# Optimization experiments

Measured on AMD Instinct MI355X. Metric: run time of the kernel, lower is better.

## Reference

```python
import jax, jax.numpy as jnp
import numpy as np
import math

B, S, D = 4, 1024, 1024
H, DK, DV = 16, 64, 64
MAX_REL = 32  # use_neg_dist=True -> vocab = 2*MAX_REL+1


def setup_inputs() -> dict:
    key = jax.random.key(0)
    ks = jax.random.split(key, 13)
    sc = 0.02
    return {
        "key": jax.random.normal(ks[0], (B, S, D), jnp.float32),
        "value": jax.random.normal(ks[1], (B, S, D), jnp.float32),
        "query": jax.random.normal(ks[2], (B, S, D), jnp.float32),
        "Wk": jax.random.normal(ks[3], (D, H * DK), jnp.float32) * sc,
        "bk": jnp.zeros((H * DK,), jnp.float32),
        "Wq": jax.random.normal(ks[4], (D, H * DK), jnp.float32) * sc,
        "bq": jnp.zeros((H * DK,), jnp.float32),
        "Wv": jax.random.normal(ks[5], (D, H * DV), jnp.float32) * sc,
        "bv": jnp.zeros((H * DV,), jnp.float32),
        "Wo": jax.random.normal(ks[6], (H * DV, D), jnp.float32) * sc,
        "bo": jnp.zeros((D,), jnp.float32),
        "emb_k": jax.random.normal(ks[7], (2 * MAX_REL + 1, DK), jnp.float32) * sc,
        "emb_v": jax.random.normal(ks[8], (2 * MAX_REL + 1, DV), jnp.float32) * sc,
    }


def reference(key, value, query, Wk, bk, Wq, bq, Wv, bv, Wo, bo, emb_k, emb_v):
    # project and split heads -> [B, H, S, d]
    def shape(x, d):
        return x.reshape(B, S, H, d).transpose(0, 2, 1, 3)

    k = shape(key @ Wk + bk, DK)
    v = shape(value @ Wv + bv, DV)
    q = shape(query @ Wq + bq, DK)

    # relative position ids: [S, S] in [0, 2*MAX_REL]
    r = jnp.arange(S)
    rel_idx = jnp.clip(r[None, :] - r[:, None], -MAX_REL, MAX_REL) + MAX_REL
    rel_k = emb_k[rel_idx]  # [S, S, DK]
    rel_v = emb_v[rel_idx]  # [S, S, DV]

    q = q / math.sqrt(DK)
    # content scores + relative-key scores (relative_matmul with transpose=True)
    scores = jnp.einsum("bhqd,bhkd->bhqk", q, k) + jnp.einsum("bhqd,qkd->bhqk", q, rel_k)
    attn = jax.nn.softmax(scores.astype(jnp.float32), axis=-1).astype(q.dtype)

    # context + relative-value contribution (relative_matmul with transpose=False)
    ctx = jnp.einsum("bhqk,bhkd->bhqd", attn, v) + jnp.einsum("bhqk,qkd->bhqd", attn, rel_v)
    ctx = ctx.transpose(0, 2, 1, 3).reshape(B, S, H * DV)
    final_output = ctx @ Wo + bo
    return final_output, attn
```

## Files before the change

kernel.cpp:

```cpp
#include <hip/hip_runtime.h>
#include <hip/hip_bf16.h>

#define B_ 4
#define S_ 1024
#define D_ 1024
#define H_ 16

typedef unsigned short u16;
typedef __bf16 bf16x8 __attribute__((ext_vector_type(8)));
typedef float f32x4 __attribute__((ext_vector_type(4)));

__device__ inline u16 f2bf(float f) {
    __bf16 h = (__bf16)f;
    return __builtin_bit_cast(u16, h);
}
__device__ inline float bf2f(u16 u) {
    unsigned int x = ((unsigned int)u) << 16;
    return __builtin_bit_cast(float, x);
}
__device__ inline void gl_lds16(const u16* g, u16* lbase) {
    __builtin_amdgcn_global_load_lds(
        (const __attribute__((address_space(1))) unsigned int*)g,
        (__attribute__((address_space(3))) unsigned int*)lbase, 16, 0, 0);
}
__device__ inline bf16x8 frag_swz(const u16* lds, int row, int chunk) {
    int off = (row << 6) + ((chunk ^ (row & 7)) << 3);
    return *(const bf16x8*)(lds + off);
}
__device__ inline bf16x8 frag_p(const u16* lds, int row, int chunk) {
    int off = row * 72 + (chunk << 3);
    return *(const bf16x8*)(lds + off);
}
__device__ inline f32x4 mfma16(bf16x8 a, bf16x8 b, f32x4 c) {
    return __builtin_amdgcn_mfma_f32_16x16x32_bf16(a, b, c, 0, 0, 0);
}
__device__ inline void bar() {
    asm volatile("s_waitcnt lgkmcnt(0)\n\ts_barrier" ::: "memory");
}
__device__ inline void wait_vm0() {
    asm volatile("s_waitcnt vmcnt(0)" ::: "memory");
    __builtin_amdgcn_sched_barrier(0);
}
__device__ inline void wait_vm4() {
    asm volatile("s_waitcnt vmcnt(4)" ::: "memory");
    __builtin_amdgcn_sched_barrier(0);
}
__device__ inline void wait_vm8() {
    asm volatile("s_waitcnt vmcnt(8)" ::: "memory");
    __builtin_amdgcn_sched_barrier(0);
}
__device__ inline void wait_vm16() {
    asm volatile("s_waitcnt vmcnt(16)" ::: "memory");
    __builtin_amdgcn_sched_barrier(0);
}
__device__ inline void wait_vm20() {
    asm volatile("s_waitcnt vmcnt(20)" ::: "memory");
    __builtin_amdgcn_sched_barrier(0);
}
__device__ inline void wait_lgkm0() {
    asm volatile("s_waitcnt lgkmcnt(0)" ::: "memory");
    __builtin_amdgcn_sched_barrier(0);
}

__global__ __launch_bounds__(256) void cast_bf16_kernel(const float* __restrict__ src,
                                                        u16* __restrict__ dst, int n) {
    int i = (blockIdx.x * 256 + threadIdx.x) * 4;
    if (i >= n) return;
    float4 v = *(const float4*)(src + i);
    ushort4 o;
    o.x = f2bf(v.x); o.y = f2bf(v.y); o.z = f2bf(v.z); o.w = f2bf(v.w);
    *(ushort4*)(dst + i) = o;
}

__global__ __launch_bounds__(256) void tcast_kernel(const float* __restrict__ src,
                                                    u16* __restrict__ dst) {
    __shared__ float tile[32][33];
    int bx = blockIdx.x, by = blockIdx.y;
    int tx = threadIdx.x, ty = threadIdx.y;
    int x = bx * 32 + tx;
    for (int i = ty; i < 32; i += 8)
        tile[i][tx] = src[(size_t)(by * 32 + i) * 1024 + x];
    __syncthreads();
    int col = by * 32 + tx;
    for (int i = ty; i < 32; i += 8)
        dst[(size_t)(bx * 32 + i) * 1024 + col] = f2bf(tile[tx][i]);
}

__device__ inline void gemm_core(const u16* __restrict__ A, const u16* __restrict__ Bt,
                                 int m0, int n0, u16* lsA, u16* lsB, f32x4 acc[4][4]) {
    int tid = threadIdx.x, lane = tid & 63, wave = tid >> 6;
    int quad = lane >> 4, l16 = lane & 15;
    int wm = wave >> 1, wn = wave & 1;
    f32x4 z = {0.0f, 0.0f, 0.0f, 0.0f};
    for (int mi = 0; mi < 4; mi++)
        for (int ni = 0; ni < 4; ni++) acc[mi][ni] = z;
    auto stg = [&](int k0, int b) {
        const u16* abase = A + (size_t)m0 * 1024 + k0;
        const u16* bbase = Bt + (size_t)n0 * 1024 + k0;
#pragma unroll
        for (int j = 0; j < 4; j++) {
            int C = (wave * 4 + j) * 64 + lane;
            int row = C >> 3, c = C & 7;
            int sw = (c ^ (row & 7)) << 3;
            gl_lds16(abase + (size_t)row * 1024 + sw, lsA + b * 8192 + (wave * 4 + j) * 512);
            gl_lds16(bbase + (size_t)row * 1024 + sw, lsB + b * 8192 + (wave * 4 + j) * 512);
        }
    };
    stg(0, 0);
#pragma unroll 1
    for (int it = 0; it < 16; it++) {
        if (it < 15) {
            stg((it + 1) * 64, (it + 1) & 1);
            wait_vm8();
        } else {
            wait_vm0();
        }
        bar();
        const u16* cA = lsA + (it & 1) * 8192;
        const u16* cB = lsB + (it & 1) * 8192;
        for (int s = 0; s < 2; s++) {
            bf16x8 af[4], bfv[4];
            for (int mi = 0; mi < 4; mi++) af[mi] = frag_swz(cA, wm * 64 + mi * 16 + l16, s * 4 + quad);
            for (int ni = 0; ni < 4; ni++) bfv[ni] = frag_swz(cB, wn * 64 + ni * 16 + l16, s * 4 + quad);
            for (int mi = 0; mi < 4; mi++)
                for (int ni = 0; ni < 4; ni++)
                    acc[mi][ni] = mfma16(af[mi], bfv[ni], acc[mi][ni]);
        }
        bar();
    }
}

__global__ __launch_bounds__(256) void gemm_proj_kernel(
    const u16* __restrict__ xq, const u16* __restrict__ xk, const u16* __restrict__ xv,
    const u16* __restrict__ wt,
    const float* __restrict__ bq, const float* __restrict__ bk, const float* __restrict__ bv,
    u16* __restrict__ qb, u16* __restrict__ kb, u16* __restrict__ vtb) {
    __shared__ __align__(16) u16 lsA[2 * 128 * 64];
    __shared__ __align__(16) u16 lsB[2 * 128 * 64];
    int bid = blockIdx.x;
    int which = bid >> 8;
    int t = bid & 255;
    int m0 = (t >> 3) * 128, n0 = (t & 7) * 128;
    const u16* A = which == 0 ? xq : (which == 1 ? xk : xv);
    const u16* Bt = wt + (size_t)which * 1024 * 1024;
    const float* bias = which == 0 ? bq : (which == 1 ? bk : bv);
    f32x4 acc[4][4];
    gemm_core(A, Bt, m0, n0, lsA, lsB, acc);
    int tid = threadIdx.x, lane = tid & 63, wave = tid >> 6;
    int quad = lane >> 4, l16 = lane & 15;
    int wm = wave >> 1, wn = wave & 1;
    for (int mi = 0; mi < 4; mi++) {
        int rbase = m0 + wm * 64 + mi * 16 + quad * 4;
        int b = rbase >> 10, s0 = rbase & 1023;
        for (int ni = 0; ni < 4; ni++) {
            int n = n0 + wn * 64 + ni * 16 + l16;
            int h = n >> 6, d = n & 63;
            float bsv = bias[n];
            if (which == 2) {
                ushort4 pk;
                pk.x = f2bf(acc[mi][ni][0] + bsv);
                pk.y = f2bf(acc[mi][ni][1] + bsv);
                pk.z = f2bf(acc[mi][ni][2] + bsv);
                pk.w = f2bf(acc[mi][ni][3] + bsv);
                *(ushort4*)(vtb + ((size_t)(b * H_ + h) * 64 + d) * 1024 + s0) = pk;
            } else {
                u16* outp = (which == 0) ? qb : kb;
                float scl = (which == 0) ? 0.125f : 1.0f;
                for (int r = 0; r < 4; r++) {
                    int s = s0 + r;
                    outp[((size_t)(b * H_ + h) * 1024 + s) * 64 + d] = f2bf((acc[mi][ni][r] + bsv) * scl);
                }
            }
        }
    }
}

__global__ __launch_bounds__(256) void gemm_final_kernel(const u16* __restrict__ ctxb,
                                                         const u16* __restrict__ wot,
                                                         const float* __restrict__ bo,
                                                         float* __restrict__ out) {
    __shared__ __align__(16) u16 lsA[2 * 128 * 64];
    __shared__ __align__(16) u16 lsB[2 * 128 * 64];
    int bid = blockIdx.x;
    int m0 = (bid >> 3) * 128, n0 = (bid & 7) * 128;
    f32x4 acc[4][4];
    gemm_core(ctxb, wot, m0, n0, lsA, lsB, acc);
    int tid = threadIdx.x, lane = tid & 63, wave = tid >> 6;
    int quad = lane >> 4, l16 = lane & 15;
    int wm = wave >> 1, wn = wave & 1;
    for (int mi = 0; mi < 4; mi++)
        for (int ni = 0; ni < 4; ni++) {
            int n = n0 + wn * 64 + ni * 16 + l16;
            float bsv = bo[n];
            for (int r = 0; r < 4; r++) {
                int row = m0 + wm * 64 + mi * 16 + quad * 4 + r;
                out[(size_t)row * 1024 + n] = acc[mi][ni][r] + bsv;
            }
        }
}

__global__ __launch_bounds__(256, 2) void attn_kernel(
    const u16* __restrict__ qb, const u16* __restrict__ kb, const u16* __restrict__ vtb,
    const float* __restrict__ emb_k, const float* __restrict__ emb_v,
    float* __restrict__ attn_out, u16* __restrict__ ctxb) {
    __shared__ __align__(16) u16 kvbuf[4][64 * 64];
    __shared__ __align__(16) u16 pbuf[64 * 72];
    __shared__ __align__(16) u16 wqbuf[64 * 72];
    __shared__ __align__(16) u16 qrel[64 * 68];

    int bid = blockIdx.x;
    int qt = bid & 15, bh = bid >> 4;
    int tid = threadIdx.x, lane = tid & 63, wave = tid >> 6;
    int quad = lane >> 4, l16 = lane & 15;
    int mrow = wave * 16;

    const u16* qbase = qb + ((size_t)bh * 1024 + qt * 64) * 64;
    const u16* kbh = kb + (size_t)bh * 1024 * 64;
    const u16* vbh = vtb + (size_t)bh * 64 * 1024;

    auto stage = [&](const u16* src, int srcStride, u16* dst) {
#pragma unroll
        for (int j = 0; j < 2; j++) {
            int C = (wave * 2 + j) * 64 + lane;
            int row = C >> 3, c = C & 7;
            gl_lds16(src + (size_t)row * srcStride + ((c ^ (row & 7)) << 3),
                     dst + (wave * 2 + j) * 512);
        }
    };
    auto stage128 = [&](const u16* src, u16* dst) {
#pragma unroll
        for (int j = 0; j < 4; j++) {
            int C = (wave * 4 + j) * 64 + lane;
            int row = C >> 3, c = C & 7;
            gl_lds16(src + (size_t)row * 64 + ((c ^ (row & 7)) << 3),
                     dst + (wave * 4 + j) * 512);
        }
    };

    stage(qbase, 64, wqbuf);
    for (int i = tid; i < 65 * 64; i += 256) {
        int j = i >> 6, d = i & 63;
        pbuf[(j << 6) + ((((d >> 3) ^ (j & 7)) << 3) | (d & 7))] = f2bf(emb_k[i]);
    }
    wait_vm0();
    bar();

    {
        bf16x8 a0 = frag_swz(wqbuf, mrow + l16, quad);
        bf16x8 a1 = frag_swz(wqbuf, mrow + l16, 4 + quad);
#pragma unroll
        for (int ni = 0; ni < 5; ni++) {
            int rr = ni * 16 + l16;
            rr = rr > 64 ? 64 : rr;
            f32x4 a = {0.0f, 0.0f, 0.0f, 0.0f};
            a = mfma16(a0, frag_swz(pbuf, rr, quad), a);
            a = mfma16(a1, frag_swz(pbuf, rr, 4 + quad), a);
            int j = ni * 16 + l16;
            if (j < 65) {
#pragma unroll
                for (int r = 0; r < 4; r++)
                    qrel[(mrow + quad * 4 + r) * 68 + j] = f2bf(a[r]);
            }
        }
    }
    bf16x8 aq0 = frag_swz(wqbuf, mrow + l16, quad);
    bf16x8 aq1 = frag_swz(wqbuf, mrow + l16, 4 + quad);
    bar();

    float rel_l[4], rel_r[4];
#pragma unroll
    for (int r = 0; r < 4; r++) {
        int ql = mrow + quad * 4 + r;
        rel_l[r] = bf2f(qrel[ql * 68 + 0]);
        rel_r[r] = bf2f(qrel[ql * 68 + 64]);
    }
    stage128(kbh, kvbuf[0]);
    {
        unsigned int* wz = (unsigned int*)wqbuf;
        for (int i = lane; i < 16 * 36; i += 64) wz[mrow * 36 + i] = 0u;
    }

    float l_acc[4] = {0.0f, 0.0f, 0.0f, 0.0f};

#pragma unroll 1
    for (int it = 0; it < 8; it++) {
        if (it < 7) {
            stage128(kbh + (size_t)(it + 1) * 8192, (it & 1) ? kvbuf[0] : kvbuf[2]);
            wait_vm4();
        } else {
            wait_vm0();
        }
        bar();
        const u16* kl = (it & 1) ? kvbuf[2] : kvbuf[0];
        int cls = (it * 128 + 127 <= qt * 64 - 32) ? 0 : ((it * 128 >= qt * 64 + 95) ? 2 : 1);
        if (cls == 0) {
#pragma unroll
            for (int ni = 0; ni < 8; ni++) {
                f32x4 a = {0.0f, 0.0f, 0.0f, 0.0f};
                a = mfma16(aq0, frag_swz(kl, ni * 16 + l16, quad), a);
                a = mfma16(aq1, frag_swz(kl, ni * 16 + l16, 4 + quad), a);
#pragma unroll
                for (int r = 0; r < 4; r++) l_acc[r] += __expf(a[r] + rel_l[r]);
            }
        } else if (cls == 2) {
#pragma unroll
            for (int ni = 0; ni < 8; ni++) {
                f32x4 a = {0.0f, 0.0f, 0.0f, 0.0f};
                a = mfma16(aq0, frag_swz(kl, ni * 16 + l16, quad), a);
                a = mfma16(aq1, frag_swz(kl, ni * 16 + l16, 4 + quad), a);
#pragma unroll
                for (int r = 0; r < 4; r++) l_acc[r] += __expf(a[r] + rel_r[r]);
            }
        } else {
#pragma unroll
            for (int ni = 0; ni < 8; ni++) {
                f32x4 a = {0.0f, 0.0f, 0.0f, 0.0f};
                a = mfma16(aq0, frag_swz(kl, ni * 16 + l16, quad), a);
                a = mfma16(aq1, frag_swz(kl, ni * 16 + l16, 4 + quad), a);
#pragma unroll
                for (int r = 0; r < 4; r++) {
                    int ql = mrow + quad * 4 + r;
                    int qg = qt * 64 + ql;
                    int kg = it * 128 + ni * 16 + l16;
                    int jj = kg - qg;
                    jj = jj < -32 ? -32 : (jj > 32 ? 32 : jj);
                    l_acc[r] += __expf(a[r] + bf2f(qrel[ql * 68 + jj + 32]));
                }
            }
        }
        bar();
    }

    float rl[4];
#pragma unroll
    for (int r = 0; r < 4; r++) {
        float l = l_acc[r];
        l += __shfl_xor(l, 1);
        l += __shfl_xor(l, 2);
        l += __shfl_xor(l, 4);
        l += __shfl_xor(l, 8);
        rl[r] = 1.0f / l;
    }
    float wl[4] = {0.0f, 0.0f, 0.0f, 0.0f};
    float wr[4] = {0.0f, 0.0f, 0.0f, 0.0f};
    f32x4 ctx[4];
    {
        f32x4 z = {0.0f, 0.0f, 0.0f, 0.0f};
#pragma unroll
        for (int ni = 0; ni < 4; ni++) ctx[ni] = z;
    }
    float* attn_bh = attn_out + (size_t)bh * 1024 * 1024;

    stage(kbh, 64, kvbuf[0]);
    stage(vbh, 1024, kvbuf[2]);
    wait_vm0();
    bar();
#pragma unroll 1
    for (int kt = 0; kt < 16; kt++) {
        if (kt < 15) {
            stage(kbh + (size_t)(kt + 1) * 4096, 64, (kt & 1) ? kvbuf[0] : kvbuf[1]);
            stage(vbh + (kt + 1) * 64, 1024, (kt & 1) ? kvbuf[2] : kvbuf[3]);
        }
        if (kt == 0) wait_vm4();
        else if (kt == 15) wait_vm16();
        else wait_vm20();
        bar();
        const u16* kl = (kt & 1) ? kvbuf[1] : kvbuf[0];
        const u16* vl = (kt & 1) ? kvbuf[3] : kvbuf[2];
        f32x4 sc[4];
#pragma unroll
        for (int ni = 0; ni < 4; ni++) {
            f32x4 a = {0.0f, 0.0f, 0.0f, 0.0f};
            a = mfma16(aq0, frag_swz(kl, ni * 16 + l16, quad), a);
            a = mfma16(aq1, frag_swz(kl, ni * 16 + l16, 4 + quad), a);
            sc[ni] = a;
        }
        int cls = (kt <= qt - 2) ? 0 : ((kt >= qt + 2) ? 2 : 1);
        if (cls == 0) {
#pragma unroll
            for (int ni = 0; ni < 4; ni++)
#pragma unroll
                for (int r = 0; r < 4; r++) {
                    int ql = mrow + quad * 4 + r;
                    int qg = qt * 64 + ql;
                    int kg = kt * 64 + ni * 16 + l16;
                    float p = __expf(sc[ni][r] + rel_l[r]) * rl[r];
                    __builtin_nontemporal_store(p, &attn_bh[(size_t)qg * 1024 + kg]);
                    pbuf[ql * 72 + ni * 16 + l16] = f2bf(p);
                    wl[r] += p;
                }
        } else if (cls == 2) {
#pragma unroll
            for (int ni = 0; ni < 4; ni++)
#pragma unroll
                for (int r = 0; r < 4; r++) {
                    int ql = mrow + quad * 4 + r;
                    int qg = qt * 64 + ql;
                    int kg = kt * 64 + ni * 16 + l16;
                    float p = __expf(sc[ni][r] + rel_r[r]) * rl[r];
                    __builtin_nontemporal_store(p, &attn_bh[(size_t)qg * 1024 + kg]);
                    pbuf[ql * 72 + ni * 16 + l16] = f2bf(p);
                    wr[r] += p;
                }
        } else {
#pragma unroll
            for (int ni = 0; ni < 4; ni++)
#pragma unroll
                for (int r = 0; r < 4; r++) {
                    int ql = mrow + quad * 4 + r;
                    int qg = qt * 64 + ql;
                    int kg = kt * 64 + ni * 16 + l16;
                    int jj = kg - qg;
                    int jc = jj < -32 ? -32 : (jj > 32 ? 32 : jj);
                    float p = __expf(sc[ni][r] + bf2f(qrel[ql * 68 + jc + 32])) * rl[r];
                    __builtin_nontemporal_store(p, &attn_bh[(size_t)qg * 1024 + kg]);
                    u16 pb = f2bf(p);
                    pbuf[ql * 72 + ni * 16 + l16] = pb;
                    if (jj <= -32) wl[r] += p;
                    else if (jj >= 32) wr[r] += p;
                    else wqbuf[ql * 72 + jj + 32] = pb;
                }
        }
        wait_lgkm0();
#pragma unroll
        for (int s2 = 0; s2 < 2; s2++) {
            bf16x8 af = frag_p(pbuf, mrow + l16, s2 * 4 + quad);
#pragma unroll
            for (int ni = 0; ni < 4; ni++)
                ctx[ni] = mfma16(af, frag_swz(vl, ni * 16 + l16, s2 * 4 + quad), ctx[ni]);
        }
        bar();
    }

#pragma unroll
    for (int r = 0; r < 4; r++) {
        wl[r] += __shfl_xor(wl[r], 1); wl[r] += __shfl_xor(wl[r], 2);
        wl[r] += __shfl_xor(wl[r], 4); wl[r] += __shfl_xor(wl[r], 8);
        wr[r] += __shfl_xor(wr[r], 1); wr[r] += __shfl_xor(wr[r], 2);
        wr[r] += __shfl_xor(wr[r], 4); wr[r] += __shfl_xor(wr[r], 8);
    }
    if (l16 == 0) {
#pragma unroll
        for (int r = 0; r < 4; r++)
            wqbuf[(mrow + quad * 4 + r) * 72] = f2bf(wl[r]);
    }
    u16* evt = kvbuf[0];
    for (int i = tid; i < 4096; i += 256) {
        int j = i >> 6, d = i & 63;
        evt[d * 72 + j] = f2bf(emb_v[i]);
    }
    __syncthreads();
#pragma unroll
    for (int s2 = 0; s2 < 2; s2++) {
        bf16x8 af = frag_p(wqbuf, mrow + l16, s2 * 4 + quad);
#pragma unroll
        for (int ni = 0; ni < 4; ni++)
            ctx[ni] = mfma16(af, frag_p(evt, ni * 16 + l16, s2 * 4 + quad), ctx[ni]);
    }
#pragma unroll
    for (int ni = 0; ni < 4; ni++) {
        float ev = emb_v[64 * 64 + ni * 16 + l16];
#pragma unroll
        for (int r = 0; r < 4; r++) ctx[ni][r] += wr[r] * ev;
    }

    int b = bh >> 4, h = bh & 15;
#pragma unroll
    for (int ni = 0; ni < 4; ni++)
#pragma unroll
        for (int r = 0; r < 4; r++) {
            int ql = mrow + quad * 4 + r;
            int sg = qt * 64 + ql;
            ctxb[((size_t)b * 1024 + sg) * 1024 + h * 64 + ni * 16 + l16] = f2bf(ctx[ni][r]);
        }
}

extern "C" void kernel_launch(void* const* d_in, const int* in_sizes, int n_in,
                              void* d_out, int out_size, void* d_ws, size_t ws_size,
                              hipStream_t stream) {
    const float* key_f   = (const float*)d_in[0];
    const float* value_f = (const float*)d_in[1];
    const float* query_f = (const float*)d_in[2];
    const float* Wk = (const float*)d_in[3];
    const float* bk = (const float*)d_in[4];
    const float* Wq = (const float*)d_in[5];
    const float* bq = (const float*)d_in[6];
    const float* Wv = (const float*)d_in[7];
    const float* bv = (const float*)d_in[8];
    const float* Wo = (const float*)d_in[9];
    const float* bo = (const float*)d_in[10];
    const float* emb_k = (const float*)d_in[11];
    const float* emb_v = (const float*)d_in[12];

    char* ws = (char*)d_ws;
    const size_t MB = 1024 * 1024;
    u16* xq   = (u16*)(ws + 0 * MB);
    u16* xk   = (u16*)(ws + 8 * MB);
    u16* xv   = (u16*)(ws + 16 * MB);
    u16* wt   = (u16*)(ws + 24 * MB);
    u16* wot  = (u16*)(ws + 30 * MB);
    u16* qb   = (u16*)(ws + 32 * MB);
    u16* kb   = (u16*)(ws + 40 * MB);
    u16* vtb  = (u16*)(ws + 48 * MB);
    u16* ctxb = (u16*)(ws + 56 * MB);

    float* out0 = (float*)d_out;
    float* attn = out0 + (size_t)4 * 1024 * 1024;

    cast_bf16_kernel<<<4096, 256, 0, stream>>>(query_f, xq, 4194304);
    cast_bf16_kernel<<<4096, 256, 0, stream>>>(key_f,   xk, 4194304);
    cast_bf16_kernel<<<4096, 256, 0, stream>>>(value_f, xv, 4194304);
    dim3 tg(32, 32), tb(32, 8);
    tcast_kernel<<<tg, tb, 0, stream>>>(Wq, wt);
    tcast_kernel<<<tg, tb, 0, stream>>>(Wk, wt + 1024 * 1024);
    tcast_kernel<<<tg, tb, 0, stream>>>(Wv, wt + 2 * 1024 * 1024);
    tcast_kernel<<<tg, tb, 0, stream>>>(Wo, wot);
    gemm_proj_kernel<<<768, 256, 0, stream>>>(xq, xk, xv, wt, bq, bk, bv, qb, kb, vtb);
    attn_kernel<<<1024, 256, 0, stream>>>(qb, kb, vtb, emb_k, emb_v, attn, ctxb);
    gemm_final_kernel<<<256, 256, 0, stream>>>(ctxb, wot, bo, out0);
}
```

Baseline: 492.8 us.

## Merge cast launches, add XCD-aware block swizzle and MFMA wave priority

```diff
diff --git a/kernel.cpp b/kernel.cpp
--- a/kernel.cpp
+++ b/kernel.cpp
@@ -23,6 +23,10 @@
         (const __attribute__((address_space(1))) unsigned int*)g,
         (__attribute__((address_space(3))) unsigned int*)lbase, 16, 0, 0);
 }
+__device__ inline int xcd_swz(int bid, int nwg) {
+    int cpx = nwg >> 3;
+    return (bid & 7) * cpx + (bid >> 3);
+}
 __device__ inline bf16x8 frag_swz(const u16* lds, int row, int chunk) {
     int off = (row << 6) + ((chunk ^ (row & 7)) << 3);
     return *(const bf16x8*)(lds + off);
@@ -62,19 +66,29 @@
     __builtin_amdgcn_sched_barrier(0);
 }
 
-__global__ __launch_bounds__(256) void cast_bf16_kernel(const float* __restrict__ src,
-                                                        u16* __restrict__ dst, int n) {
-    int i = (blockIdx.x * 256 + threadIdx.x) * 4;
-    if (i >= n) return;
-    float4 v = *(const float4*)(src + i);
+__global__ __launch_bounds__(256) void cast3_kernel(
+    const float* __restrict__ q, const float* __restrict__ k, const float* __restrict__ v,
+    u16* __restrict__ xq, u16* __restrict__ xk, u16* __restrict__ xv) {
+    int bid = blockIdx.x;
+    int which = bid >> 12;
+    int t = bid & 4095;
+    const float* src = which == 0 ? q : (which == 1 ? k : v);
+    u16* dst = which == 0 ? xq : (which == 1 ? xk : xv);
+    int i = (t * 256 + threadIdx.x) * 4;
+    float4 val = *(const float4*)(src + i);
     ushort4 o;
-    o.x = f2bf(v.x); o.y = f2bf(v.y); o.z = f2bf(v.z); o.w = f2bf(v.w);
+    o.x = f2bf(val.x); o.y = f2bf(val.y); o.z = f2bf(val.z); o.w = f2bf(val.w);
     *(ushort4*)(dst + i) = o;
 }
 
-__global__ __launch_bounds__(256) void tcast_kernel(const float* __restrict__ src,
-                                                    u16* __restrict__ dst) {
+__global__ __launch_bounds__(256) void tcast4_kernel(
+    const float* __restrict__ Wq, const float* __restrict__ Wk,
+    const float* __restrict__ Wv, const float* __restrict__ Wo,
+    u16* __restrict__ wt, u16* __restrict__ wot) {
     __shared__ float tile[32][33];
+    int z = blockIdx.z;
+    const float* src = z == 0 ? Wq : (z == 1 ? Wk : (z == 2 ? Wv : Wo));
+    u16* dst = z < 3 ? wt + (size_t)z * 1024 * 1024 : wot;
     int bx = blockIdx.x, by = blockIdx.y;
     int tx = threadIdx.x, ty = threadIdx.y;
     int x = bx * 32 + tx;
@@ -137,7 +151,7 @@
     u16* __restrict__ qb, u16* __restrict__ kb, u16* __restrict__ vtb) {
     __shared__ __align__(16) u16 lsA[2 * 128 * 64];
     __shared__ __align__(16) u16 lsB[2 * 128 * 64];
-    int bid = blockIdx.x;
+    int bid = xcd_swz(blockIdx.x, 768);
     int which = bid >> 8;
     int t = bid & 255;
     int m0 = (t >> 3) * 128, n0 = (t & 7) * 128;
@@ -181,7 +195,7 @@
                                                          float* __restrict__ out) {
     __shared__ __align__(16) u16 lsA[2 * 128 * 64];
     __shared__ __align__(16) u16 lsB[2 * 128 * 64];
-    int bid = blockIdx.x;
+    int bid = xcd_swz(blockIdx.x, 256);
     int m0 = (bid >> 3) * 128, n0 = (bid & 7) * 128;
     f32x4 acc[4][4];
     gemm_core(ctxb, wot, m0, n0, lsA, lsB, acc);
@@ -208,7 +222,7 @@
     __shared__ __align__(16) u16 wqbuf[64 * 72];
     __shared__ __align__(16) u16 qrel[64 * 68];
 
-    int bid = blockIdx.x;
+    int bid = xcd_swz(blockIdx.x, 1024);
     int qt = bid & 15, bh = bid >> 4;
     int tid = threadIdx.x, lane = tid & 63, wave = tid >> 6;
     int quad = lane >> 4, l16 = lane & 15;
@@ -293,6 +307,7 @@
         bar();
         const u16* kl = (it & 1) ? kvbuf[2] : kvbuf[0];
         int cls = (it * 128 + 127 <= qt * 64 - 32) ? 0 : ((it * 128 >= qt * 64 + 95) ? 2 : 1);
+        __builtin_amdgcn_s_setprio(1);
         if (cls == 0) {
 #pragma unroll
             for (int ni = 0; ni < 8; ni++) {
@@ -328,6 +343,7 @@
                 }
             }
         }
+        __builtin_amdgcn_s_setprio(0);
         bar();
     }
 
@@ -368,6 +384,7 @@
         const u16* kl = (kt & 1) ? kvbuf[1] : kvbuf[0];
         const u16* vl = (kt & 1) ? kvbuf[3] : kvbuf[2];
         f32x4 sc[4];
+        __builtin_amdgcn_s_setprio(1);
 #pragma unroll
         for (int ni = 0; ni < 4; ni++) {
             f32x4 a = {0.0f, 0.0f, 0.0f, 0.0f};
@@ -375,6 +392,7 @@
             a = mfma16(aq1, frag_swz(kl, ni * 16 + l16, 4 + quad), a);
             sc[ni] = a;
         }
+        __builtin_amdgcn_s_setprio(0);
         int cls = (kt <= qt - 2) ? 0 : ((kt >= qt + 2) ? 2 : 1);
         if (cls == 0) {
 #pragma unroll
@@ -422,6 +440,7 @@
                 }
         }
         wait_lgkm0();
+        __builtin_amdgcn_s_setprio(1);
 #pragma unroll
         for (int s2 = 0; s2 < 2; s2++) {
             bf16x8 af = frag_p(pbuf, mrow + l16, s2 * 4 + quad);
@@ -429,6 +448,7 @@
             for (int ni = 0; ni < 4; ni++)
                 ctx[ni] = mfma16(af, frag_swz(vl, ni * 16 + l16, s2 * 4 + quad), ctx[ni]);
         }
+        __builtin_amdgcn_s_setprio(0);
         bar();
     }
 
@@ -507,14 +527,9 @@
     float* out0 = (float*)d_out;
     float* attn = out0 + (size_t)4 * 1024 * 1024;
 
-    cast_bf16_kernel<<<4096, 256, 0, stream>>>(query_f, xq, 4194304);
-    cast_bf16_kernel<<<4096, 256, 0, stream>>>(key_f,   xk, 4194304);
-    cast_bf16_kernel<<<4096, 256, 0, stream>>>(value_f, xv, 4194304);
-    dim3 tg(32, 32), tb(32, 8);
-    tcast_kernel<<<tg, tb, 0, stream>>>(Wq, wt);
-    tcast_kernel<<<tg, tb, 0, stream>>>(Wk, wt + 1024 * 1024);
-    tcast_kernel<<<tg, tb, 0, stream>>>(Wv, wt + 2 * 1024 * 1024);
-    tcast_kernel<<<tg, tb, 0, stream>>>(Wo, wot);
+    cast3_kernel<<<12288, 256, 0, stream>>>(query_f, key_f, value_f, xq, xk, xv);
+    dim3 tg(32, 32, 4), tb(32, 8);
+    tcast4_kernel<<<tg, tb, 0, stream>>>(Wq, Wk, Wv, Wo, wt, wot);
     gemm_proj_kernel<<<768, 256, 0, stream>>>(xq, xk, xv, wt, bq, bk, bv, qb, kb, vtb);
     attn_kernel<<<1024, 256, 0, stream>>>(qb, kb, vtb, emb_k, emb_v, attn, ctxb);
     gemm_final_kernel<<<256, 256, 0, stream>>>(ctxb, wot, bo, out0);
```

New measurement: 481.5 us. -2.3%, faster.
